# Performance work log

Hardware: AMD Instinct MI355X
Metric: run time of the kernel (lower is better)

Reference implementation:

```python
import jax, jax.numpy as jnp
import numpy as np

C = 256
N, H, W = 4, 64, 64


def _conv1x1(x, w, b):
    # 1x1 Conv2d == per-pixel linear: x [N,C,H,W], w [O,C], b [O]
    return jnp.einsum('nchw,oc->nohw', x, w) + b[None, :, None, None]


def setup_inputs() -> dict:
    key = jax.random.key(0)
    ks = jax.random.split(key, 9)
    inputs = jax.random.normal(ks[0], (N, C, H, W), dtype=jnp.float32)
    scale = 1.0 / np.sqrt(C)
    d = {'inputs': inputs}
    for i in range(4):
        d[f'w{i}'] = jax.random.normal(ks[1 + 2 * i], (C, C), dtype=jnp.float32) * scale
        d[f'b{i}'] = jax.random.normal(ks[2 + 2 * i], (C,), dtype=jnp.float32) * 0.01
    return d


def reference(inputs, w0, b0, w1, b1, w2, b2, w3, b3):
    n, c, h, w = inputs.shape
    hw = h * w
    # f_v, f_k, f_q: [N, HW, C] (NCHW conv output permuted to NHWC then flattened)
    f_v = _conv1x1(inputs, w0, b0).transpose(0, 2, 3, 1).reshape(n, hw, c)
    f_k = _conv1x1(inputs, w1, b1).transpose(0, 2, 3, 1).reshape(n, hw, c)
    f_q = _conv1x1(inputs, w2, b2).transpose(0, 2, 3, 1).reshape(n, hw, c)
    # w[n,i,j] = <k_i, q_j> / HW   (no softmax)
    att = jnp.einsum('nid,njd->nij', f_k, f_q) / hw
    # f_r[n,j,c] = sum_i w[n,i,j] * v[n,i,c]  (matmul with w^T)
    f_r = jnp.einsum('nij,nic->njc', att, f_v)
    f_r = f_r.reshape(n, h, w, c).transpose(0, 3, 1, 2)  # back to NCHW
    return _conv1x1(f_r, w3, b3)
```

## Files before the change

kernel.cpp:

```cpp
#include <hip/hip_runtime.h>

#define NB 4
#define CD 256
#define HW 4096
#define KSG 16
#define CC (CD * CD)

typedef __attribute__((ext_vector_type(8))) short bf16x8;
typedef __attribute__((ext_vector_type(4))) float f32x4;

__device__ inline unsigned short f2bf(float x) {
  unsigned int u = __float_as_uint(x);
  unsigned int r = (u + 0x7FFFu + ((u >> 16) & 1u)) >> 16;
  return (unsigned short)r;
}
__device__ inline float bfhi(unsigned short h) {
  return __uint_as_float(((unsigned int)h) << 16);
}
__device__ __forceinline__ void gload16(const unsigned short* g, unsigned short* l) {
  __builtin_amdgcn_global_load_lds((const __attribute__((address_space(1))) void*)g,
                                   (__attribute__((address_space(3))) void*)l, 16, 0, 0);
}

template <int BOFF>
__device__ __forceinline__ void mfma_body(const unsigned short* sm, f32x4 acc[4][2]) {
  int t = threadIdx.x, lane = t & 63, wid = t >> 6;
  int wr = wid >> 2, wc = wid & 3;
  int lrow = lane & 15, lkb = lane >> 4;
#pragma unroll
  for (int ks2 = 0; ks2 < 2; ++ks2) {
    bf16x8 ah[4], al[4], bh[2], bl[2];
#pragma unroll
    for (int m = 0; m < 4; ++m) {
      int r = wr * 64 + m * 16 + lrow;
      int sw = ((ks2 * 4 + lkb) ^ (r & 7)) * 8;
      ah[m] = *(const bf16x8*)(sm + r * 64 + sw);
      al[m] = *(const bf16x8*)(sm + 8192 + r * 64 + sw);
    }
#pragma unroll
    for (int q = 0; q < 2; ++q) {
      int r = wc * 32 + q * 16 + lrow;
      int sw = ((ks2 * 4 + lkb) ^ (r & 7)) * 8;
      bh[q] = *(const bf16x8*)(sm + BOFF + r * 64 + sw);
      bl[q] = *(const bf16x8*)(sm + BOFF + 8192 + r * 64 + sw);
    }
#pragma unroll
    for (int m = 0; m < 4; ++m)
#pragma unroll
      for (int q = 0; q < 2; ++q) {
        acc[m][q] = __builtin_amdgcn_mfma_f32_16x16x32_bf16(ah[m], bh[q], acc[m][q], 0, 0, 0);
        acc[m][q] = __builtin_amdgcn_mfma_f32_16x16x32_bf16(ah[m], bl[q], acc[m][q], 0, 0, 0);
        acc[m][q] = __builtin_amdgcn_mfma_f32_16x16x32_bf16(al[m], bh[q], acc[m][q], 0, 0, 0);
      }
  }
}

__device__ __forceinline__ void mfma_nt_core(
    const unsigned short* __restrict__ pH, const unsigned short* __restrict__ pL,
    const unsigned short* __restrict__ qH, const unsigned short* __restrict__ qL,
    int i0, int j0, unsigned short* sm, f32x4 acc[4][2]) {
  int t = threadIdx.x;
  int lane = t & 63, wid = t >> 6;
  int tsel = wid >> 1;
  int gbase = (wid & 1) * 8;
  const unsigned short* bp2 = (tsel == 0) ? pH : (tsel == 1) ? pL : (tsel == 2) ? qH : qL;
  int tb = (tsel < 2) ? i0 : j0;
  int rsub = lane >> 3;
  int gc = (lane & 7) ^ rsub;
  unsigned short* ldsT = sm + tsel * 8192;
#pragma unroll
  for (int m = 0; m < 4; ++m)
#pragma unroll
    for (int q = 0; q < 2; ++q) acc[m][q] = (f32x4){0.f, 0.f, 0.f, 0.f};
  for (int k0 = 0; k0 < 256; k0 += 64) {
#pragma unroll
    for (int s = 0; s < 8; ++s) {
      int g = gbase + s;
      gload16(bp2 + (size_t)(tb + g * 8 + rsub) * CD + k0 + gc * 8, ldsT + g * 512);
    }
    __syncthreads();
    mfma_body<16384>(sm, acc);
    __syncthreads();
  }
}

template <bool DIAG>
__device__ __forceinline__ void gram_core(const float* __restrict__ Xn, int i0, int j0,
                                          int kBegin, unsigned short* sm,
                                          f32x4 acc[4][2], float* __restrict__ psumRow) {
  int t = threadIdx.x;
  int r16 = t >> 4, k4 = (t & 15) * 4;
  int kg = k4 >> 3, kr = k4 & 7;
#pragma unroll
  for (int m = 0; m < 4; ++m)
#pragma unroll
    for (int q = 0; q < 2; ++q) acc[m][q] = (f32x4){0.f, 0.f, 0.f, 0.f};
  float ps[4] = {0.f, 0.f, 0.f, 0.f};
  float4 av[4], bv[4];
#pragma unroll
  for (int j = 0; j < 4; ++j) {
    av[j] = *(const float4*)(Xn + (size_t)(i0 + j * 32 + r16) * HW + kBegin + k4);
    if (!DIAG)
      bv[j] = *(const float4*)(Xn + (size_t)(j0 + j * 32 + r16) * HW + kBegin + k4);
  }
#pragma unroll
  for (int s = 0; s < 4; ++s) {
    float4 av2[4], bv2[4];
    if (s < 3) {
#pragma unroll
      for (int j = 0; j < 4; ++j) {
        av2[j] = *(const float4*)(Xn + (size_t)(i0 + j * 32 + r16) * HW + kBegin +
                                  (s + 1) * 64 + k4);
        if (!DIAG)
          bv2[j] = *(const float4*)(Xn + (size_t)(j0 + j * 32 + r16) * HW + kBegin +
                                    (s + 1) * 64 + k4);
      }
    }
#pragma unroll
    for (int j = 0; j < 4; ++j) {
      int r = j * 32 + r16;
      int off = r * 64 + ((kg ^ (r & 7)) << 3) + kr;
      ushort4 h, l;
      h.x = f2bf(av[j].x); l.x = f2bf(av[j].x - bfhi(h.x));
      h.y = f2bf(av[j].y); l.y = f2bf(av[j].y - bfhi(h.y));
      h.z = f2bf(av[j].z); l.z = f2bf(av[j].z - bfhi(h.z));
      h.w = f2bf(av[j].w); l.w = f2bf(av[j].w - bfhi(h.w));
      *(ushort4*)(sm + off) = h;
      *(ushort4*)(sm + 8192 + off) = l;
      ps[j] += av[j].x + av[j].y + av[j].z + av[j].w;
      if (!DIAG) {
        h.x = f2bf(bv[j].x); l.x = f2bf(bv[j].x - bfhi(h.x));
        h.y = f2bf(bv[j].y); l.y = f2bf(bv[j].y - bfhi(h.y));
        h.z = f2bf(bv[j].z); l.z = f2bf(bv[j].z - bfhi(h.z));
        h.w = f2bf(bv[j].w); l.w = f2bf(bv[j].w - bfhi(h.w));
        *(ushort4*)(sm + 16384 + off) = h;
        *(ushort4*)(sm + 24576 + off) = l;
      }
    }
    __syncthreads();
    mfma_body<DIAG ? 0 : 16384>(sm, acc);
    __syncthreads();
    if (s < 3) {
#pragma unroll
      for (int j = 0; j < 4; ++j) {
        av[j] = av2[j];
        if (!DIAG) bv[j] = bv2[j];
      }
    }
  }
  if (psumRow) {
#pragma unroll
    for (int j = 0; j < 4; ++j) {
      float v = ps[j];
      v += __shfl_xor(v, 1); v += __shfl_xor(v, 2);
      v += __shfl_xor(v, 4); v += __shfl_xor(v, 8);
      if ((t & 15) == 0) psumRow[j * 32 + r16] = v;
    }
  }
}

__device__ __forceinline__ void stage_rowA(const float* __restrict__ W, int ld, int r0,
                                           int k0, unsigned short* dst) {
  int t = threadIdx.x;
  int r16 = t >> 4, k4 = (t & 15) * 4;
  int kg = k4 >> 3, kr = k4 & 7;
#pragma unroll
  for (int j = 0; j < 4; ++j) {
    int r = j * 32 + r16;
    float4 v = *(const float4*)(W + (size_t)(r0 + r) * ld + k0 + k4);
    int off = r * 64 + ((kg ^ (r & 7)) << 3) + kr;
    ushort4 h, l;
    h.x = f2bf(v.x); l.x = f2bf(v.x - bfhi(h.x));
    h.y = f2bf(v.y); l.y = f2bf(v.y - bfhi(h.y));
    h.z = f2bf(v.z); l.z = f2bf(v.z - bfhi(h.z));
    h.w = f2bf(v.w); l.w = f2bf(v.w - bfhi(h.w));
    *(ushort4*)(dst + off) = h;
    *(ushort4*)(dst + 8192 + off) = l;
  }
}

__device__ __forceinline__ void stage_colT(const float* __restrict__ W, int ld, int c0,
                                           int k0, unsigned short* dst) {
  int t = threadIdx.x;
#pragma unroll
  for (int ee = 0; ee < 8; ++ee) {
    int flat = ee * 512 + t;
    int c2 = flat >> 7, p = flat & 127;
    const float* src = W + (size_t)(k0 + 2 * c2) * ld + c0 + p;
    float xa = src[0], xb = src[ld];
    int c = 2 * c2;
    int off = p * 64 + ((((c >> 3)) ^ (p & 7)) << 3) + (c & 7);
    unsigned short ha = f2bf(xa), hb = f2bf(xb);
    ushort2 hv; hv.x = ha; hv.y = hb;
    ushort2 lv; lv.x = f2bf(xa - bfhi(ha)); lv.y = f2bf(xb - bfhi(hb));
    *(ushort2*)(dst + off) = hv;
    *(ushort2*)(dst + 8192 + off) = lv;
  }
}

__device__ __forceinline__ void final_core(const unsigned short* __restrict__ aH,
                                           const unsigned short* __restrict__ aL,
                                           const float* __restrict__ Xn, int i0, int j0,
                                           unsigned short* sm, f32x4 acc[4][2]) {
  int t = threadIdx.x, lane = t & 63, wid = t >> 6;
  const unsigned short* ap = (wid & 4) ? aL : aH;
  unsigned short* ldsA = sm + ((wid & 4) ? 8192 : 0);
  int rsub = lane >> 3;
  int gc = (lane & 7) ^ rsub;
  int gq = wid & 3;
#pragma unroll
  for (int m = 0; m < 4; ++m)
#pragma unroll
    for (int q = 0; q < 2; ++q) acc[m][q] = (f32x4){0.f, 0.f, 0.f, 0.f};
  float xa[8], xb[8];
#pragma unroll
  for (int s2 = 0; s2 < 4; ++s2) {
    int g = gq * 4 + s2;
    gload16(ap + (size_t)(i0 + g * 8 + rsub) * CD + gc * 8, ldsA + g * 512);
  }
#pragma unroll
  for (int ee = 0; ee < 8; ++ee) {
    int flat = ee * 512 + t;
    int c2 = flat >> 7, p = flat & 127;
    const float* src = Xn + (size_t)(2 * c2) * HW + j0 + p;
    xa[ee] = src[0];
    xb[ee] = src[HW];
  }
#pragma unroll
  for (int s = 0; s < 4; ++s) {
#pragma unroll
    for (int ee = 0; ee < 8; ++ee) {
      int flat = ee * 512 + t;
      int c2 = flat >> 7, p = flat & 127;
      int c = 2 * c2;
      int off = p * 64 + ((((c >> 3)) ^ (p & 7)) << 3) + (c & 7);
      unsigned short ha = f2bf(xa[ee]), hb = f2bf(xb[ee]);
      ushort2 hv; hv.x = ha; hv.y = hb;
      ushort2 lv; lv.x = f2bf(xa[ee] - bfhi(ha)); lv.y = f2bf(xb[ee] - bfhi(hb));
      *(ushort2*)(sm + 16384 + off) = hv;
      *(ushort2*)(sm + 24576 + off) = lv;
    }
    float xa2[8], xb2[8];
    if (s < 3) {
#pragma unroll
      for (int ee = 0; ee < 8; ++ee) {
        int flat = ee * 512 + t;
        int c2 = flat >> 7, p = flat & 127;
        const float* src = Xn + (size_t)((s + 1) * 64 + 2 * c2) * HW + j0 + p;
        xa2[ee] = src[0];
        xb2[ee] = src[HW];
      }
    }
    __syncthreads();
    mfma_body<16384>(sm, acc);
    __syncthreads();
    if (s < 3) {
#pragma unroll
      for (int s2 = 0; s2 < 4; ++s2) {
        int g = gq * 4 + s2;
        gload16(ap + (size_t)(i0 + g * 8 + rsub) * CD + (s + 1) * 64 + gc * 8,
                ldsA + g * 512);
      }
#pragma unroll
      for (int ee = 0; ee < 8; ++ee) { xa[ee] = xa2[ee]; xb[ee] = xb2[ee]; }
    }
  }
}

__device__ __forceinline__ void epi_store(f32x4 acc[4][2], float* smf, float* dst,
                                          int ld, const float* cvrow) {
  int t = threadIdx.x, lane = t & 63, wid = t >> 6;
  int wr = wid >> 2, wc = wid & 3;
#pragma unroll
  for (int m = 0; m < 4; ++m) {
    int rbase = wr * 64 + m * 16 + ((lane >> 4) << 2);
#pragma unroll
    for (int q = 0; q < 2; ++q) {
      int col = wc * 32 + q * 16 + (lane & 15);
#pragma unroll
      for (int e = 0; e < 4; ++e) {
        int row = rbase + e;
        smf[row * 128 + (col ^ ((row & 4) << 2))] = acc[m][q][e];
      }
    }
  }
  __syncthreads();
#pragma unroll
  for (int it = 0; it < 8; ++it) {
    int row = it * 16 + wid * 2 + (lane >> 5);
    int col = (lane & 31) * 4;
    float4 v = *(const float4*)&smf[row * 128 + (col ^ ((row & 4) << 2))];
    if (cvrow) {
      float cb = cvrow[row];
      v.x += cb; v.y += cb; v.z += cb; v.w += cb;
    }
    *(float4*)(dst + (size_t)row * ld + col) = v;
  }
}

__global__ __launch_bounds__(512) void kB(
    const float* __restrict__ X, float* __restrict__ Gp, float* __restrict__ psum2,
    const float* __restrict__ w0, const float* __restrict__ w1,
    const float* __restrict__ w2, const float* __restrict__ w3,
    const float* __restrict__ b0, const float* __restrict__ b1,
    const float* __restrict__ b2, unsigned short* __restrict__ Eh,
    unsigned short* __restrict__ El, float* __restrict__ Et,
    unsigned short* __restrict__ Fth, unsigned short* __restrict__ Ftl,
    float* __restrict__ Ff, float* __restrict__ vp, float* __restrict__ bpv,
    float* __restrict__ dlt, float* __restrict__ scal1) {
  __shared__ __align__(16) unsigned short sm[32768];
  int x = blockIdx.x, t = threadIdx.x;
  if (x < 192) {
    int tile = x % 3;
    int z = x / 3;
    int n = z >> 4, ks = z & 15;
    const float* Xn = X + (size_t)n * CD * HW;
    f32x4 acc[4][2];
    if (tile == 1) {
      gram_core<false>(Xn, 0, 128, ks * 256, sm, acc, nullptr);
      epi_store(acc, (float*)sm, Gp + ((size_t)ks * NB + n) * CC + 128, CD, nullptr);
    } else {
      int i0 = (tile == 2) ? 128 : 0;
      float* psRow = psum2 + ((size_t)n * 16 + ks) * 256 + i0;
      gram_core<true>(Xn, i0, i0, ks * 256, sm, acc, psRow);
      epi_store(acc, (float*)sm,
                Gp + ((size_t)ks * NB + n) * CC + (size_t)i0 * CD + i0, CD, nullptr);
    }
  } else if (x < 200) {
    int e = x - 192;
    int zc = e >> 2, q = e & 3;
    int i0 = (q >> 1) * 128, j0 = (q & 1) * 128;
    f32x4 acc[4][2];
#pragma unroll
    for (int m = 0; m < 4; ++m)
#pragma unroll
      for (int qq = 0; qq < 2; ++qq) acc[m][qq] = (f32x4){0.f, 0.f, 0.f, 0.f};
    for (int s = 0; s < 4; ++s) {
      int k0 = s * 64;
      if (zc == 0) stage_rowA(w3, CD, i0, k0, sm);
      else stage_colT(w2, CD, i0, k0, sm);
      stage_colT(zc ? w1 : w0, CD, j0, k0, sm + 16384);
      __syncthreads();
      mfma_body<16384>(sm, acc);
      __syncthreads();
    }
    unsigned short* oh = zc ? Fth : Eh;
    unsigned short* ol = zc ? Ftl : El;
    float* tf = zc ? Ff : Et;
    int lane = t & 63, wid = t >> 6, wr = wid >> 2, wc = wid & 3;
#pragma unroll
    for (int m = 0; m < 4; ++m) {
      int row = i0 + wr * 64 + m * 16 + ((lane >> 4) << 2);
#pragma unroll
      for (int q2 = 0; q2 < 2; ++q2) {
        int col = j0 + wc * 32 + q2 * 16 + (lane & 15);
#pragma unroll
        for (int e2 = 0; e2 < 4; ++e2) {
          float v = acc[m][q2][e2];
          unsigned short hh = f2bf(v), ll = f2bf(v - bfhi(hh));
          oh[(size_t)(row + e2) * CD + col] = hh;
          ol[(size_t)(row + e2) * CD + col] = ll;
          tf[(size_t)col * CD + row + e2] = v;
        }
      }
    }
  } else {
    int task = x - 200;
    if (task < 8) {
      float* vin = (float*)sm;
      int seg = task & 3;
      const float* Wm = (task < 4) ? w1 : w2;
      const float* v = (task < 4) ? b2 : b1;
      float* dst = (task < 4) ? (vp + seg * CD) : (bpv + seg * CD);
      if (t < 64) vin[t] = v[seg * 64 + t];
      __syncthreads();
      if (t < 256) {
        float a = 0.f;
#pragma unroll 16
        for (int kk = 0; kk < 64; ++kk)
          a += Wm[(size_t)(seg * 64 + kk) * CD + t] * vin[kk];
        dst[t] = a;
      }
    } else if (task < 12) {
      int lane = t & 63, wv = t >> 6;
      float4 bvv = *(const float4*)(b0 + lane * 4);
#pragma unroll
      for (int i = 0; i < 8; ++i) {
        int o = (task - 8) * 64 + wv * 8 + i;
        float4 v = *(const float4*)(w3 + (size_t)o * CD + lane * 4);
        float a = v.x * bvv.x + v.y * bvv.y + v.z * bvv.z + v.w * bvv.w;
        a += __shfl_xor(a, 1);  a += __shfl_xor(a, 2);  a += __shfl_xor(a, 4);
        a += __shfl_xor(a, 8);  a += __shfl_xor(a, 16); a += __shfl_xor(a, 32);
        if (lane == 0) dlt[o] = a;
      }
    } else if (task == 12) {
      float* red = (float*)sm;
      if (t < 256) red[t] = b1[t] * b2[t];
      __syncthreads();
      for (int off = 128; off > 0; off >>= 1) {
        if (t < off) red[t] += red[t + off];
        __syncthreads();
      }
      if (t == 0) scal1[0] = red[0];
    }
  }
}

__global__ __launch_bounds__(512) void kC(
    const float* __restrict__ Gp, float* __restrict__ G,
    unsigned short* __restrict__ Gh, unsigned short* __restrict__ Gl,
    const float* __restrict__ psum2, const float* __restrict__ vp,
    const float* __restrict__ Ff, const float* __restrict__ Et,
    float* __restrict__ alp, float* __restrict__ gam, float* __restrict__ scal0) {
  __shared__ float smf[512];
  int b = blockIdx.x, t = threadIdx.x;
  if (b < 96) {
#pragma unroll
    for (int s = 0; s < 4; ++s) {
      int f = b * 2048 + s * 512 + t;
      int b2 = f >> 8, tt = f & 255;
      int quad = b2 >> 8, r = b2 & 255, n = r >> 6;
      int idx = (r & 63) * 256 + tt;
      int i = (idx >> 7) + ((quad == 2) ? 128 : 0);
      int j = (idx & 127) + ((quad >= 1) ? 128 : 0);
      float a = 0.f;
#pragma unroll
      for (int ks = 0; ks < KSG; ++ks)
        a += Gp[((size_t)ks * NB + n) * CC + (size_t)i * CD + j];
      size_t o = (size_t)n * CC + (size_t)i * CD + j;
      unsigned short hh = f2bf(a), ll = f2bf(a - bfhi(hh));
      G[o] = a; Gh[o] = hh; Gl[o] = ll;
      if (quad == 1) {
        size_t o2 = (size_t)n * CC + (size_t)j * CD + i;
        G[o2] = a; Gh[o2] = hh; Gl[o2] = ll;
      }
    }
  } else {
    int n = b - 96;
    float* ss = smf;
    float* red = ss + 256;
    float a = 0.f;
    if (t < 256) {
#pragma unroll
      for (int ks = 0; ks < 16; ++ks) a += psum2[((size_t)n * 16 + ks) * 256 + t];
      ss[t] = a;
      red[t] = a * (vp[t] + vp[CD + t] + vp[2 * CD + t] + vp[3 * CD + t]);
    }
    __syncthreads();
    for (int off = 128; off > 0; off >>= 1) {
      if (t < off) red[t] += red[t + off];
      __syncthreads();
    }
    if (t == 0) scal0[n] = red[0];
    if (t < 256) {
      float al = 0.f, ga = 0.f;
#pragma unroll 16
      for (int k = 0; k < CD; ++k) {
        float sk = ss[k];
        al += Ff[(size_t)k * CD + t] * sk;
        ga += Et[(size_t)k * CD + t] * sk;
      }
      alp[n * CD + t] = al;
      gam[n * CD + t] = ga;
    }
  }
}

__global__ __launch_bounds__(512) void kD1(
    const unsigned short* __restrict__ Eh, const unsigned short* __restrict__ El,
    const unsigned short* __restrict__ Gh, const unsigned short* __restrict__ Gl,
    unsigned short* __restrict__ Rh, unsigned short* __restrict__ Rl,
    const float* __restrict__ G, const float* __restrict__ Et,
    const float* __restrict__ vp, const float* __restrict__ dlt,
    const float* __restrict__ gam, const float* __restrict__ scal0,
    const float* __restrict__ scal1, const float* __restrict__ b3,
    float* __restrict__ cv) {
  __shared__ __align__(16) unsigned short sm[32768];
  int b = blockIdx.x, t = threadIdx.x;
  if (b < 16) {
    int n = b >> 2, i0 = ((b >> 1) & 1) * 128, j0 = (b & 1) * 128;
    f32x4 acc[4][2];
    mfma_nt_core(Eh, El, Gh + (size_t)n * CC, Gl + (size_t)n * CC, i0, j0, sm, acc);
    int lane = t & 63, wid = t >> 6, wr = wid >> 2, wc = wid & 3;
#pragma unroll
    for (int m = 0; m < 4; ++m) {
      int row = i0 + wr * 64 + m * 16 + ((lane >> 4) << 2);
#pragma unroll
      for (int q = 0; q < 2; ++q) {
        int col = j0 + wc * 32 + q * 16 + (lane & 15);
#pragma unroll
        for (int e = 0; e < 4; ++e) {
          float v = acc[m][q][e];
          unsigned short hh = f2bf(v), ll = f2bf(v - bfhi(hh));
          Rh[(size_t)n * CC + (size_t)(row + e) * CD + col] = hh;
          Rl[(size_t)n * CC + (size_t)(row + e) * CD + col] = ll;
        }
      }
    }
  } else {
    int n = b - 16;
    float* vsh = (float*)sm;
    float* g1 = vsh + CD;
    if (t < CD) vsh[t] = vp[t] + vp[CD + t] + vp[2 * CD + t] + vp[3 * CD + t];
    __syncthreads();
    if (t < CD) {
      const float* Gn = G + (size_t)n * CC;
      float a = 0.f;
#pragma unroll 8
      for (int k = 0; k < CD; ++k) a += Gn[(size_t)k * CD + t] * vsh[k];
      g1[t] = a;
    }
    __syncthreads();
    if (t < CD) {
      float c2 = 0.f;
#pragma unroll 8
      for (int k = 0; k < CD; ++k) c2 += Et[(size_t)k * CD + t] * g1[k];
      cv[n * CD + t] = (c2 + scal0[n] * dlt[t] +
                        scal1[0] * (gam[n * CD + t] + (float)HW * dlt[t])) *
                           (1.0f / HW) +
                       b3[t];
    }
  }
}

__global__ __launch_bounds__(512) void kD2(
    const unsigned short* __restrict__ Rh, const unsigned short* __restrict__ Rl,
    const unsigned short* __restrict__ Fth, const unsigned short* __restrict__ Ftl,
    unsigned short* __restrict__ Athi, unsigned short* __restrict__ Atlo,
    const float* __restrict__ dlt, const float* __restrict__ alp,
    const float* __restrict__ gam, const float* __restrict__ bpv) {
  __shared__ __align__(16) unsigned short sm[32768];
  int b = blockIdx.x, t = threadIdx.x;
  int n = b >> 2, i0 = ((b >> 1) & 1) * 128, j0 = (b & 1) * 128;
  f32x4 acc[4][2];
  mfma_nt_core(Rh + (size_t)n * CC, Rl + (size_t)n * CC, Fth, Ftl, i0, j0, sm, acc);
  int lane = t & 63, wid = t >> 6, wr = wid >> 2, wc = wid & 3;
#pragma unroll
  for (int m = 0; m < 4; ++m) {
    int row = i0 + wr * 64 + m * 16 + ((lane >> 4) << 2);
#pragma unroll
    for (int q = 0; q < 2; ++q) {
      int col = j0 + wc * 32 + q * 16 + (lane & 15);
      float bj = bpv[col] + bpv[CD + col] + bpv[2 * CD + col] + bpv[3 * CD + col];
      float aj = alp[n * CD + col];
#pragma unroll
      for (int e = 0; e < 4; ++e) {
        float di = dlt[row + e], gi = gam[n * CD + row + e];
        float v = (acc[m][q][e] + di * aj + gi * bj) * (1.0f / HW) + di * bj;
        unsigned short hh = f2bf(v), ll = f2bf(v - bfhi(hh));
        Athi[(size_t)n * CC + (size_t)(row + e) * CD + col] = hh;
        Atlo[(size_t)n * CC + (size_t)(row + e) * CD + col] = ll;
      }
    }
  }
}

__global__ __launch_bounds__(512) void kF(const unsigned short* __restrict__ Athi,
                                          const unsigned short* __restrict__ Atlo,
                                          const float* __restrict__ X,
                                          const float* __restrict__ cv,
                                          float* __restrict__ out) {
  int n = blockIdx.z;
  int i0 = blockIdx.x * 128, j0 = blockIdx.y * 128;
  __shared__ __align__(16) unsigned short sm[32768];
  f32x4 acc[4][2];
  final_core(Athi + (size_t)n * CC, Atlo + (size_t)n * CC, X + (size_t)n * CD * HW, i0,
             j0, sm, acc);
  epi_store(acc, (float*)sm, out + (size_t)n * CD * HW + (size_t)i0 * HW + j0, HW,
            cv + n * CD + i0);
}

extern "C" void kernel_launch(void* const* d_in, const int* in_sizes, int n_in,
                              void* d_out, int out_size, void* d_ws, size_t ws_size,
                              hipStream_t stream) {
  const float* X = (const float*)d_in[0];
  const float* w0 = (const float*)d_in[1];
  const float* b0 = (const float*)d_in[2];
  const float* w1 = (const float*)d_in[3];
  const float* b1 = (const float*)d_in[4];
  const float* w2 = (const float*)d_in[5];
  const float* b2 = (const float*)d_in[6];
  const float* w3 = (const float*)d_in[7];
  const float* b3 = (const float*)d_in[8];
  float* out = (float*)d_out;
  float* ws = (float*)d_ws;

  float* cv    = ws;
  float* alp   = ws + 1024;
  float* gam   = ws + 2048;
  float* dlt   = ws + 3072;
  float* vp    = ws + 4096;
  float* bpv   = ws + 5120;
  float* scal0 = ws + 6144;
  float* scal1 = ws + 6176;
  float* psum2 = ws + 8192;
  float* Et    = psum2 + 16384;
  float* Ff    = Et + CC;
  float* G     = Ff + CC;
  float* Gp    = G + (size_t)NB * CC;
  unsigned short* Eh   = (unsigned short*)(Gp + (size_t)KSG * NB * CC);
  unsigned short* El   = Eh + CC;
  unsigned short* Fth  = El + CC;
  unsigned short* Ftl  = Fth + CC;
  unsigned short* Gh   = Ftl + CC;
  unsigned short* Gl   = Gh + (size_t)NB * CC;
  unsigned short* Rh   = Gl + (size_t)NB * CC;
  unsigned short* Rl   = Rh + (size_t)NB * CC;
  unsigned short* Athi = Rl + (size_t)NB * CC;
  unsigned short* Atlo = Athi + (size_t)NB * CC;

  kB<<<dim3(213), 512, 0, stream>>>(X, Gp, psum2, w0, w1, w2, w3, b0, b1, b2, Eh, El,
                                    Et, Fth, Ftl, Ff, vp, bpv, dlt, scal1);
  kC<<<dim3(100), 512, 0, stream>>>(Gp, G, Gh, Gl, psum2, vp, Ff, Et, alp, gam, scal0);
  kD1<<<dim3(20), 512, 0, stream>>>(Eh, El, Gh, Gl, Rh, Rl, G, Et, vp, dlt, gam, scal0,
                                    scal1, b3, cv);
  kD2<<<dim3(16), 512, 0, stream>>>(Rh, Rl, Fth, Ftl, Athi, Atlo, dlt, alp, gam, bpv);
  kF<<<dim3(2, 32, NB), 512, 0, stream>>>(Athi, Atlo, X, cv, out);
}
```

Baseline: 73.34 us.

## Retile final GEMM to full 256-row A tiles and double Gram K-splits

The final kernel now gives each block all 256 output channels over a 32-pixel strip, with a new MFMA body and epilogue, so each block reads X once instead of twice across two row tiles. The Gram split-K is doubled from 16 to 32 slices, giving kB more blocks with half the K work each, and the reduction loops are resized to match. The cost is more partial-sum traffic for kC to reduce, a larger LDS footprint in kF, and reloading the whole 256x256 A matrix per block.

```diff
diff --git a/kernel.cpp b/kernel.cpp
--- a/kernel.cpp
+++ b/kernel.cpp
@@ -3,7 +3,7 @@
 #define NB 4
 #define CD 256
 #define HW 4096
-#define KSG 16
+#define KSG 32
 #define CC (CD * CD)
 
 typedef __attribute__((ext_vector_type(8))) short bf16x8;
@@ -84,7 +84,7 @@
   }
 }
 
-template <bool DIAG>
+template <bool DIAG, int NSTEP>
 __device__ __forceinline__ void gram_core(const float* __restrict__ Xn, int i0, int j0,
                                           int kBegin, unsigned short* sm,
                                           f32x4 acc[4][2], float* __restrict__ psumRow) {
@@ -104,9 +104,9 @@
       bv[j] = *(const float4*)(Xn + (size_t)(j0 + j * 32 + r16) * HW + kBegin + k4);
   }
 #pragma unroll
-  for (int s = 0; s < 4; ++s) {
+  for (int s = 0; s < NSTEP; ++s) {
     float4 av2[4], bv2[4];
-    if (s < 3) {
+    if (s < NSTEP - 1) {
 #pragma unroll
       for (int j = 0; j < 4; ++j) {
         av2[j] = *(const float4*)(Xn + (size_t)(i0 + j * 32 + r16) * HW + kBegin +
@@ -140,7 +140,7 @@
     __syncthreads();
     mfma_body<DIAG ? 0 : 16384>(sm, acc);
     __syncthreads();
-    if (s < 3) {
+    if (s < NSTEP - 1) {
 #pragma unroll
       for (int j = 0; j < 4; ++j) {
         av[j] = av2[j];
@@ -198,30 +198,61 @@
   }
 }
 
-__device__ __forceinline__ void final_core(const unsigned short* __restrict__ aH,
-                                           const unsigned short* __restrict__ aL,
-                                           const float* __restrict__ Xn, int i0, int j0,
-                                           unsigned short* sm, f32x4 acc[4][2]) {
+__device__ __forceinline__ void mfma_body_kf(const unsigned short* sm, f32x4 acc[2][2]) {
+  int t = threadIdx.x, lane = t & 63, wid = t >> 6;
+  int lrow = lane & 15, lkb = lane >> 4;
+#pragma unroll
+  for (int ks2 = 0; ks2 < 2; ++ks2) {
+    bf16x8 ah[2], al[2], bh[2], bl[2];
+#pragma unroll
+    for (int m = 0; m < 2; ++m) {
+      int r = wid * 32 + m * 16 + lrow;
+      int sw = ((ks2 * 4 + lkb) ^ (r & 7)) * 8;
+      ah[m] = *(const bf16x8*)(sm + r * 64 + sw);
+      al[m] = *(const bf16x8*)(sm + 16384 + r * 64 + sw);
+    }
+#pragma unroll
+    for (int q = 0; q < 2; ++q) {
+      int p = q * 16 + lrow;
+      int sw = ((ks2 * 4 + lkb) ^ (p & 7)) * 8;
+      bh[q] = *(const bf16x8*)(sm + 32768 + p * 64 + sw);
+      bl[q] = *(const bf16x8*)(sm + 34816 + p * 64 + sw);
+    }
+#pragma unroll
+    for (int m = 0; m < 2; ++m)
+#pragma unroll
+      for (int q = 0; q < 2; ++q) {
+        acc[m][q] = __builtin_amdgcn_mfma_f32_16x16x32_bf16(ah[m], bh[q], acc[m][q], 0, 0, 0);
+        acc[m][q] = __builtin_amdgcn_mfma_f32_16x16x32_bf16(ah[m], bl[q], acc[m][q], 0, 0, 0);
+        acc[m][q] = __builtin_amdgcn_mfma_f32_16x16x32_bf16(al[m], bh[q], acc[m][q], 0, 0, 0);
+      }
+  }
+}
+
+__device__ __forceinline__ void final_core256(const unsigned short* __restrict__ aH,
+                                              const unsigned short* __restrict__ aL,
+                                              const float* __restrict__ Xn, int j0,
+                                              unsigned short* sm, f32x4 acc[2][2]) {
   int t = threadIdx.x, lane = t & 63, wid = t >> 6;
   const unsigned short* ap = (wid & 4) ? aL : aH;
-  unsigned short* ldsA = sm + ((wid & 4) ? 8192 : 0);
+  unsigned short* ldsA = sm + ((wid & 4) ? 16384 : 0);
   int rsub = lane >> 3;
   int gc = (lane & 7) ^ rsub;
   int gq = wid & 3;
 #pragma unroll
-  for (int m = 0; m < 4; ++m)
+  for (int m = 0; m < 2; ++m)
 #pragma unroll
     for (int q = 0; q < 2; ++q) acc[m][q] = (f32x4){0.f, 0.f, 0.f, 0.f};
-  float xa[8], xb[8];
-#pragma unroll
-  for (int s2 = 0; s2 < 4; ++s2) {
-    int g = gq * 4 + s2;
-    gload16(ap + (size_t)(i0 + g * 8 + rsub) * CD + gc * 8, ldsA + g * 512);
-  }
-#pragma unroll
-  for (int ee = 0; ee < 8; ++ee) {
+  float xa[2], xb[2];
+#pragma unroll
+  for (int s2 = 0; s2 < 8; ++s2) {
+    int g = gq * 8 + s2;
+    gload16(ap + (size_t)(g * 8 + rsub) * CD + gc * 8, ldsA + g * 512);
+  }
+#pragma unroll
+  for (int ee = 0; ee < 2; ++ee) {
     int flat = ee * 512 + t;
-    int c2 = flat >> 7, p = flat & 127;
+    int c2 = flat >> 5, p = flat & 31;
     const float* src = Xn + (size_t)(2 * c2) * HW + j0 + p;
     xa[ee] = src[0];
     xb[ee] = src[HW];
@@ -229,40 +260,39 @@
 #pragma unroll
   for (int s = 0; s < 4; ++s) {
 #pragma unroll
-    for (int ee = 0; ee < 8; ++ee) {
+    for (int ee = 0; ee < 2; ++ee) {
       int flat = ee * 512 + t;
-      int c2 = flat >> 7, p = flat & 127;
+      int c2 = flat >> 5, p = flat & 31;
       int c = 2 * c2;
       int off = p * 64 + ((((c >> 3)) ^ (p & 7)) << 3) + (c & 7);
       unsigned short ha = f2bf(xa[ee]), hb = f2bf(xb[ee]);
       ushort2 hv; hv.x = ha; hv.y = hb;
       ushort2 lv; lv.x = f2bf(xa[ee] - bfhi(ha)); lv.y = f2bf(xb[ee] - bfhi(hb));
-      *(ushort2*)(sm + 16384 + off) = hv;
-      *(ushort2*)(sm + 24576 + off) = lv;
-    }
-    float xa2[8], xb2[8];
+      *(ushort2*)(sm + 32768 + off) = hv;
+      *(ushort2*)(sm + 34816 + off) = lv;
+    }
+    float xa2[2], xb2[2];
     if (s < 3) {
 #pragma unroll
-      for (int ee = 0; ee < 8; ++ee) {
+      for (int ee = 0; ee < 2; ++ee) {
         int flat = ee * 512 + t;
-        int c2 = flat >> 7, p = flat & 127;
+        int c2 = flat >> 5, p = flat & 31;
         const float* src = Xn + (size_t)((s + 1) * 64 + 2 * c2) * HW + j0 + p;
         xa2[ee] = src[0];
         xb2[ee] = src[HW];
       }
     }
     __syncthreads();
-    mfma_body<16384>(sm, acc);
+    mfma_body_kf(sm, acc);
     __syncthreads();
     if (s < 3) {
 #pragma unroll
-      for (int s2 = 0; s2 < 4; ++s2) {
-        int g = gq * 4 + s2;
-        gload16(ap + (size_t)(i0 + g * 8 + rsub) * CD + (s + 1) * 64 + gc * 8,
-                ldsA + g * 512);
-      }
-#pragma unroll
-      for (int ee = 0; ee < 8; ++ee) { xa[ee] = xa2[ee]; xb[ee] = xb2[ee]; }
+      for (int s2 = 0; s2 < 8; ++s2) {
+        int g = gq * 8 + s2;
+        gload16(ap + (size_t)(g * 8 + rsub) * CD + (s + 1) * 64 + gc * 8, ldsA + g * 512);
+      }
+#pragma unroll
+      for (int ee = 0; ee < 2; ++ee) { xa[ee] = xa2[ee]; xb[ee] = xb2[ee]; }
     }
   }
 }
@@ -295,6 +325,33 @@
       v.x += cb; v.y += cb; v.z += cb; v.w += cb;
     }
     *(float4*)(dst + (size_t)row * ld + col) = v;
+  }
+}
+
+__device__ __forceinline__ void epi_store256(f32x4 acc[2][2], float* smf, float* dst,
+                                             const float* cvrow) {
+  int t = threadIdx.x, lane = t & 63, wid = t >> 6;
+#pragma unroll
+  for (int m = 0; m < 2; ++m) {
+#pragma unroll
+    for (int q = 0; q < 2; ++q) {
+      int col = q * 16 + (lane & 15);
+#pragma unroll
+      for (int e = 0; e < 4; ++e) {
+        int row = wid * 32 + m * 16 + ((lane >> 4) << 2) + e;
+        smf[row * 36 + col] = acc[m][q][e];
+      }
+    }
+  }
+  __syncthreads();
+#pragma unroll
+  for (int it = 0; it < 4; ++it) {
+    int slot = it * 512 + t;
+    int row = slot >> 3, col = (slot & 7) * 4;
+    float4 v = *(const float4*)&smf[row * 36 + col];
+    float cb = cvrow[row];
+    v.x += cb; v.y += cb; v.z += cb; v.w += cb;
+    *(float4*)(dst + (size_t)row * HW + col) = v;
   }
 }
 
@@ -310,24 +367,24 @@
     float* __restrict__ dlt, float* __restrict__ scal1) {
   __shared__ __align__(16) unsigned short sm[32768];
   int x = blockIdx.x, t = threadIdx.x;
-  if (x < 192) {
+  if (x < 384) {
     int tile = x % 3;
     int z = x / 3;
-    int n = z >> 4, ks = z & 15;
+    int n = z >> 5, ks = z & 31;
     const float* Xn = X + (size_t)n * CD * HW;
     f32x4 acc[4][2];
     if (tile == 1) {
-      gram_core<false>(Xn, 0, 128, ks * 256, sm, acc, nullptr);
+      gram_core<false, 2>(Xn, 0, 128, ks * 128, sm, acc, nullptr);
       epi_store(acc, (float*)sm, Gp + ((size_t)ks * NB + n) * CC + 128, CD, nullptr);
     } else {
       int i0 = (tile == 2) ? 128 : 0;
-      float* psRow = psum2 + ((size_t)n * 16 + ks) * 256 + i0;
-      gram_core<true>(Xn, i0, i0, ks * 256, sm, acc, psRow);
+      float* psRow = psum2 + ((size_t)n * KSG + ks) * 256 + i0;
+      gram_core<true, 2>(Xn, i0, i0, ks * 128, sm, acc, psRow);
       epi_store(acc, (float*)sm,
                 Gp + ((size_t)ks * NB + n) * CC + (size_t)i0 * CD + i0, CD, nullptr);
     }
-  } else if (x < 200) {
-    int e = x - 192;
+  } else if (x < 392) {
+    int e = x - 384;
     int zc = e >> 2, q = e & 3;
     int i0 = (q >> 1) * 128, j0 = (q & 1) * 128;
     f32x4 acc[4][2];
@@ -365,7 +422,7 @@
       }
     }
   } else {
-    int task = x - 200;
+    int task = x - 392;
     if (task < 8) {
       float* vin = (float*)sm;
       int seg = task & 3;
@@ -424,7 +481,7 @@
       int i = (idx >> 7) + ((quad == 2) ? 128 : 0);
       int j = (idx & 127) + ((quad >= 1) ? 128 : 0);
       float a = 0.f;
-#pragma unroll
+#pragma unroll 8
       for (int ks = 0; ks < KSG; ++ks)
         a += Gp[((size_t)ks * NB + n) * CC + (size_t)i * CD + j];
       size_t o = (size_t)n * CC + (size_t)i * CD + j;
@@ -441,8 +498,8 @@
     float* red = ss + 256;
     float a = 0.f;
     if (t < 256) {
-#pragma unroll
-      for (int ks = 0; ks < 16; ++ks) a += psum2[((size_t)n * 16 + ks) * 256 + t];
+#pragma unroll 8
+      for (int ks = 0; ks < KSG; ++ks) a += psum2[((size_t)n * KSG + ks) * 256 + t];
       ss[t] = a;
       red[t] = a * (vp[t] + vp[CD + t] + vp[2 * CD + t] + vp[3 * CD + t]);
     }
@@ -560,14 +617,13 @@
                                           const float* __restrict__ X,
                                           const float* __restrict__ cv,
                                           float* __restrict__ out) {
-  int n = blockIdx.z;
-  int i0 = blockIdx.x * 128, j0 = blockIdx.y * 128;
-  __shared__ __align__(16) unsigned short sm[32768];
-  f32x4 acc[4][2];
-  final_core(Athi + (size_t)n * CC, Atlo + (size_t)n * CC, X + (size_t)n * CD * HW, i0,
-             j0, sm, acc);
-  epi_store(acc, (float*)sm, out + (size_t)n * CD * HW + (size_t)i0 * HW + j0, HW,
-            cv + n * CD + i0);
+  int n = blockIdx.y;
+  int j0 = blockIdx.x * 32;
+  __shared__ __align__(16) unsigned short sm[36864];
+  f32x4 acc[2][2];
+  final_core256(Athi + (size_t)n * CC, Atlo + (size_t)n * CC, X + (size_t)n * CD * HW,
+                j0, sm, acc);
+  epi_store256(acc, (float*)sm, out + (size_t)n * CD * HW + j0, cv + n * CD);
 }
 
 extern "C" void kernel_launch(void* const* d_in, const int* in_sizes, int n_in,
@@ -594,7 +650,7 @@
   float* scal0 = ws + 6144;
   float* scal1 = ws + 6176;
   float* psum2 = ws + 8192;
-  float* Et    = psum2 + 16384;
+  float* Et    = psum2 + 32768;
   float* Ff    = Et + CC;
   float* G     = Ff + CC;
   float* Gp    = G + (size_t)NB * CC;
@@ -609,11 +665,11 @@
   unsigned short* Athi = Rl + (size_t)NB * CC;
   unsigned short* Atlo = Athi + (size_t)NB * CC;
 
-  kB<<<dim3(213), 512, 0, stream>>>(X, Gp, psum2, w0, w1, w2, w3, b0, b1, b2, Eh, El,
+  kB<<<dim3(405), 512, 0, stream>>>(X, Gp, psum2, w0, w1, w2, w3, b0, b1, b2, Eh, El,
                                     Et, Fth, Ftl, Ff, vp, bpv, dlt, scal1);
   kC<<<dim3(100), 512, 0, stream>>>(Gp, G, Gh, Gl, psum2, vp, Ff, Et, alp, gam, scal0);
   kD1<<<dim3(20), 512, 0, stream>>>(Eh, El, Gh, Gl, Rh, Rl, G, Et, vp, dlt, gam, scal0,
                                     scal1, b3, cv);
   kD2<<<dim3(16), 512, 0, stream>>>(Rh, Rl, Fth, Ftl, Athi, Atlo, dlt, alp, gam, bpv);
-  kF<<<dim3(2, 32, NB), 512, 0, stream>>>(Athi, Atlo, X, cv, out);
-}
+  kF<<<dim3(HW / 32, NB), 512, 0, stream>>>(Athi, Atlo, X, cv, out);
+}
```

Result: slower. 86.49 us (+17.9%).
